# Performance work log

Measured on AMD Instinct MI355X. Metric: run time of the kernel, lower is better.

Reference implementation:

```python
import jax, jax.numpy as jnp
import numpy as np

IMG = 16          # imageSize
H = IMG * IMG     # hidden = num_pixels = 256
B = 32768         # batch
LAYERS = 30       # recurrent iterations


def _build_fixed_params():
    """Grid 4-neighbor adjacency + neighbor-count weights (0.25/0.34/0.5)."""
    idx = np.arange(H).reshape(IMG, IMG)
    W = np.zeros((H, H), np.float32)
    for di, dj in ((-1, 0), (1, 0), (0, -1), (0, 1)):
        src = idx[max(0, di):IMG + min(0, di), max(0, dj):IMG + min(0, dj)]
        dst = idx[max(0, -di):IMG + min(0, -di), max(0, -dj):IMG + min(0, -dj)]
        W[src.ravel(), dst.ravel()] = 1.0
    ii, jj = np.meshgrid(np.arange(IMG), np.arange(IMG), indexing='ij')
    on_edge = (ii == 0) | (ii == IMG - 1) | (jj == 0) | (jj == IMG - 1)
    corner = ((ii == 0) | (ii == IMG - 1)) & ((jj == 0) | (jj == IMG - 1))
    w = np.full(H, 0.25, np.float32)
    w[on_edge.ravel()] = 0.34
    w[corner.ravel()] = 0.5
    return W, w


def setup_inputs() -> dict:
    key = jax.random.key(0)
    k1, k2 = jax.random.split(key)
    W_np, w_np = _build_fixed_params()
    return {
        "X": jax.random.normal(k1, (B, H), dtype=jnp.float32),
        "pred": jax.random.normal(k2, (B, H), dtype=jnp.float32),
        "W_hidden": jnp.asarray(W_np),          # [H,H] fixed grid adjacency
        "w": jnp.asarray(w_np),                  # [H] per-row neighbor weight
        "a": jnp.full((H,), 1.0, jnp.float32),   # input gain (inputWeight is identity)
        "bias": jnp.full((H,), -0.15, jnp.float32),
        "scalar": jnp.full((1,), 20.0, jnp.float32),
    }


def reference(X, pred, W_hidden, w, a, bias, scalar):
    # u_fix: initial hidden with -1 entries zeroed (kept fixed across iterations)
    u_fix = jnp.where(pred == -1.0, 0.0, pred)
    Ww = w[:, None] * W_hidden                   # row-scaled adjacency [H,H]
    # inputWeight is the identity matrix, so (a*I) @ x == a * x elementwise
    drive = u_fix + bias[None, :] + a[None, :] * X   # constant per iteration [B,H]

    def step(u, _):
        v = drive + u @ Ww.T                     # [B,H]
        return jnp.tanh(v * scalar), None

    u, _ = jax.lax.scan(step, pred, None, length=LAYERS)
    return u
```

## Files before the change

kernel.cpp:

```cpp
#include <hip/hip_runtime.h>


namespace {

constexpr int HPIX   = 256;
constexpr int LAYERS = 30;
constexpr int WAVES_PER_BLOCK = 4;
constexpr int IMGS_PER_WAVE   = 2;

template <int CTRL>
__device__ __forceinline__ float dppf(float x) {
    int r = __builtin_amdgcn_update_dpp(0, __float_as_int(x), CTRL, 0xF, 0xF, true);
    return __int_as_float(r);
}

__global__ __launch_bounds__(WAVES_PER_BLOCK * 64)
void pp_kernel(const float* __restrict__ X, const float* __restrict__ pred,
               const float* __restrict__ w, const float* __restrict__ av,
               const float* __restrict__ bias, const float* __restrict__ scalar,
               float* __restrict__ out, int nb)
{
    const int lane = threadIdx.x & 63;
    const int wid  = blockIdx.x * WAVES_PER_BLOCK + (threadIdx.x >> 6);
    const int g    = lane >> 5;
    const int rg   = (lane >> 4) & 1;
    const int c    = lane & 15;
    const int img  = wid * IMGS_PER_WAVE + g;
    const bool active = (img < nb);
    const int imgc = active ? img : 0;
    const int r0   = rg * 8;
    const size_t base = (size_t)imgc * HPIX + r0 * 16 + c;

    const float s = scalar[0];
    const float K = 2.0f * s * 1.4426950408889634f;

    float u[8], drv[8];
#pragma unroll
    for (int k = 0; k < 8; ++k) {
        const int p = r0 * 16 + k * 16 + c;
        const float pr = pred[base + k * 16];
        const float x  = X[base + k * 16];
        const float fu = (pr == -1.0f) ? 0.0f : pr;
        drv[k] = K * ((fu + bias[p]) + av[p] * x);
        u[k]   = pr;
    }
    const float wEnd = K * w[c];
    const float wMid = K * w[16 + c];
    const float w_k0 = rg ? wMid : wEnd;
    const float w_k7 = rg ? wEnd : wMid;

    const int partner_addr = (lane ^ 16) << 2;

#pragma unroll 1
    for (int it = 0; it < LAYERS; ++it) {
        const float pub = rg ? u[0] : u[7];
        const float nbr = __int_as_float(
            __builtin_amdgcn_ds_bpermute(partner_addr, __float_as_int(pub)));
        const float tN = rg ? nbr : 0.0f;
        const float bN = rg ? 0.0f : nbr;

        float ns[8];
        ns[0] = tN + u[1];
        ns[7] = u[6] + bN;
#pragma unroll
        for (int k = 1; k < 7; ++k) ns[k] = u[k - 1] + u[k + 1];
#pragma unroll
        for (int k = 0; k < 8; ++k)
            ns[k] = ns[k] + dppf<0x111>(u[k]) + dppf<0x101>(u[k]);
#pragma unroll
        for (int k = 0; k < 8; ++k) {
            const float wc = (k == 0) ? w_k0 : (k == 7) ? w_k7 : wMid;
            const float m  = __builtin_fmaf(wc, ns[k], drv[k]);
            const float e  = __builtin_amdgcn_exp2f(m);
            const float rd = __builtin_amdgcn_rcpf(e + 1.0f);
            u[k] = __builtin_fmaf(rd, -2.0f, 1.0f);
        }
    }

    if (active) {
#pragma unroll
        for (int k = 0; k < 8; ++k)
            out[base + k * 16] = u[k];
    }
}

}

extern "C" void kernel_launch(void* const* d_in, const int* in_sizes, int n_in,
                              void* d_out, int out_size, void* d_ws, size_t ws_size,
                              hipStream_t stream) {
    const float* X      = (const float*)d_in[0];
    const float* pred   = (const float*)d_in[1];
    const float* w      = (const float*)d_in[3];
    const float* av     = (const float*)d_in[4];
    const float* bias   = (const float*)d_in[5];
    const float* scalar = (const float*)d_in[6];
    float* out = (float*)d_out;

    const int nb = in_sizes[0] / HPIX;
    const int imgs_per_block = WAVES_PER_BLOCK * IMGS_PER_WAVE;
    const int blocks = (nb + imgs_per_block - 1) / imgs_per_block;

    pp_kernel<<<dim3(blocks), dim3(WAVES_PER_BLOCK * 64), 0, stream>>>(
        X, pred, w, av, bias, scalar, out, nb);
}
```

Baseline: 73.27 us.

## Pack two images per lane with float2 math and Newton reciprocal tanh

Each lane now processes two images using two-wide float vectors, so the stencil and activation arithmetic can map to packed FP32 instructions. The tanh evaluation switches to exp2 of the negative absolute value, a Newton-Raphson reciprocal seeded by a linear guess, and a copysign, replacing the hardware rcp. The goal is to cut VALU issue cost per element and avoid the transcendental reciprocal. In exchange, register pressure roughly doubles and the grid has half as many waves.

Result: slower. 90.20 us (+23.1%).

```diff
diff --git a/kernel.cpp b/kernel.cpp
--- a/kernel.cpp
+++ b/kernel.cpp
@@ -6,12 +6,30 @@
 constexpr int HPIX   = 256;
 constexpr int LAYERS = 30;
 constexpr int WAVES_PER_BLOCK = 4;
-constexpr int IMGS_PER_WAVE   = 2;
+constexpr int IMGS_PER_WAVE   = 4;
+
+typedef float v2f __attribute__((ext_vector_type(2)));
 
 template <int CTRL>
 __device__ __forceinline__ float dppf(float x) {
     int r = __builtin_amdgcn_update_dpp(0, __float_as_int(x), CTRL, 0xF, 0xF, true);
     return __int_as_float(r);
+}
+
+__device__ __forceinline__ v2f act(v2f ns, v2f drv, v2f wc) {
+    const v2f m = wc * ns + drv;
+    v2f e;
+    e.x = __builtin_amdgcn_exp2f(-__builtin_fabsf(m.x));
+    e.y = __builtin_amdgcn_exp2f(-__builtin_fabsf(m.y));
+    const v2f d = e + 1.0f;
+    v2f r = e * (-8.0f / 17.0f) + (16.0f / 17.0f);
+    r = r * (2.0f - d * r);
+    r = r * (2.0f - d * r);
+    const v2f t = 1.0f - 2.0f * (e * r);
+    v2f u;
+    u.x = __builtin_copysignf(t.x, m.x);
+    u.y = __builtin_copysignf(t.y, m.y);
+    return u;
 }
 
 __global__ __launch_bounds__(WAVES_PER_BLOCK * 64)
@@ -25,62 +43,77 @@
     const int g    = lane >> 5;
     const int rg   = (lane >> 4) & 1;
     const int c    = lane & 15;
-    const int img  = wid * IMGS_PER_WAVE + g;
-    const bool active = (img < nb);
-    const int imgc = active ? img : 0;
-    const int r0   = rg * 8;
-    const size_t base = (size_t)imgc * HPIX + r0 * 16 + c;
+    const int imgA = wid * IMGS_PER_WAVE + g * 2;
+    const bool actA = (imgA < nb);
+    const bool actB = (imgA + 1 < nb);
+    const int iA = actA ? imgA : 0;
+    const int iB = actB ? imgA + 1 : 0;
+    const int r0 = rg * 8;
+    const size_t baseA = (size_t)iA * HPIX + r0 * 16 + c;
+    const size_t baseB = (size_t)iB * HPIX + r0 * 16 + c;
 
     const float s = scalar[0];
     const float K = 2.0f * s * 1.4426950408889634f;
 
-    float u[8], drv[8];
+    v2f u[8], drv[8];
 #pragma unroll
     for (int k = 0; k < 8; ++k) {
         const int p = r0 * 16 + k * 16 + c;
-        const float pr = pred[base + k * 16];
-        const float x  = X[base + k * 16];
-        const float fu = (pr == -1.0f) ? 0.0f : pr;
-        drv[k] = K * ((fu + bias[p]) + av[p] * x);
-        u[k]   = pr;
+        const float pa = pred[baseA + k * 16];
+        const float pb = pred[baseB + k * 16];
+        const float xa = X[baseA + k * 16];
+        const float xb = X[baseB + k * 16];
+        const float bk = bias[p];
+        const float ak = av[p];
+        const float fa = (pa == -1.0f) ? 0.0f : pa;
+        const float fb = (pb == -1.0f) ? 0.0f : pb;
+        drv[k].x = K * ((fa + bk) + ak * xa);
+        drv[k].y = K * ((fb + bk) + ak * xb);
+        u[k].x = pa;
+        u[k].y = pb;
     }
     const float wEnd = K * w[c];
     const float wMid = K * w[16 + c];
-    const float w_k0 = rg ? wMid : wEnd;
-    const float w_k7 = rg ? wEnd : wMid;
+    const float wk0s = rg ? wMid : wEnd;
+    const float wk7s = rg ? wEnd : wMid;
+    const v2f w_k0 = {wk0s, wk0s};
+    const v2f w_k7 = {wk7s, wk7s};
+    const v2f w_md = {wMid, wMid};
 
     const int partner_addr = (lane ^ 16) << 2;
+    const v2f vzero = {0.0f, 0.0f};
 
 #pragma unroll 1
     for (int it = 0; it < LAYERS; ++it) {
-        const float pub = rg ? u[0] : u[7];
-        const float nbr = __int_as_float(
-            __builtin_amdgcn_ds_bpermute(partner_addr, __float_as_int(pub)));
-        const float tN = rg ? nbr : 0.0f;
-        const float bN = rg ? 0.0f : nbr;
+        const v2f pub = rg ? u[0] : u[7];
+        v2f nbr;
+        nbr.x = __int_as_float(
+            __builtin_amdgcn_ds_bpermute(partner_addr, __float_as_int(pub.x)));
+        nbr.y = __int_as_float(
+            __builtin_amdgcn_ds_bpermute(partner_addr, __float_as_int(pub.y)));
+        const v2f tN = rg ? nbr : vzero;
+        const v2f bN = rg ? vzero : nbr;
 
-        float ns[8];
+        v2f ns[8];
         ns[0] = tN + u[1];
         ns[7] = u[6] + bN;
 #pragma unroll
         for (int k = 1; k < 7; ++k) ns[k] = u[k - 1] + u[k + 1];
 #pragma unroll
-        for (int k = 0; k < 8; ++k)
-            ns[k] = ns[k] + dppf<0x111>(u[k]) + dppf<0x101>(u[k]);
+        for (int k = 0; k < 8; ++k) {
+            ns[k].x += dppf<0x111>(u[k].x) + dppf<0x101>(u[k].x);
+            ns[k].y += dppf<0x111>(u[k].y) + dppf<0x101>(u[k].y);
+        }
+        u[0] = act(ns[0], drv[0], w_k0);
 #pragma unroll
-        for (int k = 0; k < 8; ++k) {
-            const float wc = (k == 0) ? w_k0 : (k == 7) ? w_k7 : wMid;
-            const float m  = __builtin_fmaf(wc, ns[k], drv[k]);
-            const float e  = __builtin_amdgcn_exp2f(m);
-            const float rd = __builtin_amdgcn_rcpf(e + 1.0f);
-            u[k] = __builtin_fmaf(rd, -2.0f, 1.0f);
-        }
+        for (int k = 1; k < 7; ++k) u[k] = act(ns[k], drv[k], w_md);
+        u[7] = act(ns[7], drv[7], w_k7);
     }
 
-    if (active) {
 #pragma unroll
-        for (int k = 0; k < 8; ++k)
-            out[base + k * 16] = u[k];
+    for (int k = 0; k < 8; ++k) {
+        if (actA) out[baseA + k * 16] = u[k].x;
+        if (actB) out[baseB + k * 16] = u[k].y;
     }
 }
 
```
